# Kernel tuning notes

Measured on AMD Instinct MI355X. Metric: run time of the kernel, lower is better.

Reference implementation:

```python
import jax, jax.numpy as jnp
import numpy as np

RADII = (0.4, 0.8, 1.2)
SIGMA2 = 2.0 * 0.2 ** 2   # Gaussian shell-density bandwidth
ALPHA = 0.3               # keras LeakyReLU default
EPS = 1e-3                # keras BatchNormalization default epsilon


def _n_coeffs(L):
    return sum((2 * l + 1) ** 2 for l in range(L + 1))


def _pullback_idx(L):
    # flat index of Wigner block entry (m, n=0) for each SH coeff (l, m)
    idx, off = [], 0
    for l in range(L + 1):
        d = 2 * l + 1
        idx += [off + m * d + l for m in range(d)]
        off += d * d
    return np.asarray(idx, dtype=np.int32)


def setup_inputs() -> dict:
    key = jax.random.key(0)
    ks = jax.random.split(key, 20)
    B, N, Q, S = 64, 2048, 1024, 512
    T = [_n_coeffs(l) for l in (5, 4, 3)]  # 286, 165, 84
    f32 = jnp.float32

    def nrm(k, shape, scale=1.0):
        return jax.random.normal(ks[k], shape, dtype=f32) * scale

    dirs = nrm(1, (3, S, 3))
    dirs = dirs / jnp.linalg.norm(dirs, axis=-1, keepdims=True)
    z = lambda n: jnp.zeros((n,), f32)
    o = lambda n: jnp.ones((n,), f32)
    return {
        "x": nrm(0, (B, N, 3)),
        "shell_dirs": dirs,                                   # [3, 512, 3]
        "A_sh": nrm(2, (36, S), 1.0 / np.sqrt(S)),            # SH projection (l_max=5)
        "D_eval0": nrm(3, (Q, T[0]), 1.0 / np.sqrt(T[0])),    # Wigner eval bases
        "D_eval1": nrm(4, (Q, T[1]), 1.0 / np.sqrt(T[1])),
        "D_eval2": nrm(5, (Q, T[2]), 1.0 / np.sqrt(T[2])),
        "D_coef1": nrm(6, (T[1], Q), 1.0 / np.sqrt(Q)),       # Wigner coeff (projection) bases
        "D_coef2": nrm(7, (T[2], Q), 1.0 / np.sqrt(Q)),
        "D_coef_last": nrm(8, (T[2], Q), 1.0 / np.sqrt(Q)),
        "W0": nrm(9, (3, 16), 1.0 / np.sqrt(3)), "b0": z(16),
        "W1": nrm(10, (16, 32), 0.25), "b1": z(32),
        "W2": nrm(11, (32, 64), 1.0 / np.sqrt(32)), "b2": z(64),
        "g0": o(16), "be0": z(16),
        "g1": o(32), "be1": z(32),
        "g2": o(64), "be2": z(64),
        "Wfc1": nrm(12, (256, 512), 1.0 / 16.0), "bfc1": z(512),
        "gfc1": o(512), "befc1": z(512),
        "Wfc2": nrm(13, (512, 256), 1.0 / np.sqrt(512)), "bfc2": z(256),
        "gfc2": o(256), "befc2": z(256),
        "Wout": nrm(14, (256, 40), 1.0 / 16.0), "bout": z(40),
    }


def _bn(y, g, b, axes):
    m = jnp.mean(y, axis=axes, keepdims=True)
    v = jnp.var(y, axis=axes, keepdims=True)
    return (y - m) * jax.lax.rsqrt(v + EPS) * g + b


def reference(x, shell_dirs, A_sh, D_eval0, D_eval1, D_eval2,
              D_coef1, D_coef2, D_coef_last,
              W0, b0, W1, b1, W2, b2,
              g0, be0, g1, be1, g2, be2,
              Wfc1, bfc1, gfc1, befc1, Wfc2, bfc2, gfc2, befc2,
              Wout, bout):
    B = x.shape[0]
    # --- sphere_shell_embedding: Gaussian shell density -> SH coeffs per shell ---
    xn2 = jnp.sum(x * x, -1)[..., None]                 # [B,N,1]
    sh = []
    for i, r in enumerate(RADII):
        c = r * shell_dirs[i]                           # [S,3]
        d2 = xn2 + jnp.sum(c * c, -1) - 2.0 * (x @ c.T)  # [B,N,S]
        f = jnp.mean(jnp.exp(-d2 / SIGMA2), axis=1)      # [B,S]
        sh.append(f @ A_sh.T)                            # [B,36]
    sh = jnp.stack(sh, axis=-1)                          # [B,36,3] shells as channels
    # --- S2_to_SO3_pullback: Y_lm -> D^l_{m,0} column of Wigner blocks ---
    idx = jnp.asarray(_pullback_idx(5))
    y = jnp.zeros((B, 286, 3), sh.dtype).at[:, idx, :].set(sh)
    # --- layer 0: SO3Conv (per-coeff channel mix) + WignerEval + BN + LReLU + WignerCoeffs ---
    y = jnp.einsum('btc,cu->btu', y, W0) + b0
    y = jnp.einsum('qt,btu->bqu', D_eval0, y)            # [B,1024,16]
    y = jax.nn.leaky_relu(_bn(y, g0, be0, (0, 1)), ALPHA)
    y = jnp.einsum('tq,bqu->btu', D_coef1, y)            # [B,165,16]
    # --- layer 1 ---
    y = jnp.einsum('btc,cu->btu', y, W1) + b1
    y = jnp.einsum('qt,btu->bqu', D_eval1, y)            # [B,1024,32]
    y = jax.nn.leaky_relu(_bn(y, g1, be1, (0, 1)), ALPHA)
    y = jnp.einsum('tq,bqu->btu', D_coef2, y)            # [B,84,32]
    # --- layer 2 ---
    y = jnp.einsum('btc,cu->btu', y, W2) + b2
    y = jnp.einsum('qt,btu->bqu', D_eval2, y)            # [B,1024,64]
    y = jax.nn.leaky_relu(_bn(y, g2, be2, (0, 1)), ALPHA)
    y = jnp.einsum('tq,bqu->btu', D_coef_last, y)        # [B,84,64]
    # --- degree-wise norms (rotation-invariant pooling), l_max=3 blocks ---
    offs, sizes = (0, 1, 10, 35), (1, 9, 25, 49)
    feats = jnp.concatenate(
        [jnp.linalg.norm(y[:, o:o + s, :], axis=1, keepdims=True)
         for o, s in zip(offs, sizes)], axis=1)          # [B,4,64]
    h = feats.reshape(B, -1)                             # [B,256]
    # --- MLP head (dropout = identity at inference) ---
    h = jax.nn.relu(_bn(h @ Wfc1 + bfc1, gfc1, befc1, (0,)))
    h = jax.nn.relu(_bn(h @ Wfc2 + bfc2, gfc2, befc2, (0,)))
    return jax.nn.softmax(h @ Wout + bout, axis=-1)
```

## Files before the change

### kernel.cpp

```cpp
#include <hip/hip_runtime.h>
#include <hip/hip_bf16.h>

#define BB 64
#define NN 2048
#define QQ 1024
#define SS 512
#define NCH 8
#define PREPB 609
#define QKN3 4

__device__ const int PIDX[36] = {
    0, 2, 5, 8, 12, 17, 22, 27, 32, 38, 45, 52, 59, 66, 73, 80,
    88, 97, 106, 115, 124, 133, 142, 151, 160,
    170, 181, 192, 203, 214, 225, 236, 247, 258, 269, 280};

__global__ __launch_bounds__(256) void k_preshell(
    const float* __restrict__ De0, const float* __restrict__ De1, const float* __restrict__ De2,
    float* __restrict__ Dg0t, float* __restrict__ rs0,
    float* __restrict__ Det1, float* __restrict__ Det2,
    float* __restrict__ stats,
    const float* __restrict__ x, const float* __restrict__ dirs, float* __restrict__ pbuf) {
    __shared__ float tile[32][33];
    __shared__ float4 lx[NN / NCH];
    int blk = blockIdx.x, tid = threadIdx.x;
    if (blk < PREPB) {
        int r = tid >> 5, c = tid & 31;
        if (blk < 192) {
            int tq = blk & 31, tt = blk >> 5;
            int q0 = tq * 32, t0 = tt * 32;
            for (int rr = r; rr < 32; rr += 8) {
                int t = t0 + c;
                tile[rr][c] = (t < 165) ? De1[(q0 + rr) * 165 + t] : 0.f;
            }
            __syncthreads();
            for (int rr = r; rr < 32; rr += 8) {
                int t = t0 + rr;
                if (t < 165) Det1[t * QQ + q0 + c] = tile[c][rr];
            }
        } else if (blk < 288) {
            int i = blk - 192;
            int tq = i & 31, tt = i >> 5;
            int q0 = tq * 32, t0 = tt * 32;
            for (int rr = r; rr < 32; rr += 8) {
                int t = t0 + c;
                tile[rr][c] = (t < 84) ? De2[(q0 + rr) * 84 + t] : 0.f;
            }
            __syncthreads();
            for (int rr = r; rr < 32; rr += 8) {
                int t = t0 + rr;
                if (t < 84) Det2[t * QQ + q0 + c] = tile[c][rr];
            }
        } else if (blk < 352) {
            int i = blk - 288;
            int tq = i & 31, tj = i >> 5;
            int q0 = tq * 32, j0 = tj * 32;
            for (int rr = r; rr < 32; rr += 8) {
                int j = j0 + c;
                tile[rr][c] = (j < 36) ? De0[(q0 + rr) * 286 + PIDX[j]] : 0.f;
            }
            __syncthreads();
            for (int rr = r; rr < 32; rr += 8) {
                int j = j0 + rr;
                if (j < 36) Dg0t[j * QQ + q0 + c] = tile[c][rr];
            }
        } else if (blk < 608) {
            int w = tid >> 6, lane = tid & 63;
            int q = (blk - 352) * 4 + w;
            float s = 0.f;
#pragma unroll
            for (int p = 0; p < 5; p++) {
                int idx = lane + p * 64;
                if (idx < 286) s += De0[q * 286 + idx];
            }
#pragma unroll
            for (int o = 32; o > 0; o >>= 1) s += __shfl_xor(s, o, 64);
            if (lane == 0) rs0[q] = s;
        } else {
            if (tid < 224) stats[tid] = 0.f;
        }
        return;
    }
    int s = blk - PREPB;
    int b = s & 63, rest = s >> 6;
    int shell = rest % 3, zc = rest / 3;
    const float KL = 18.033688011112042f;
    const float* xb = x + ((size_t)b * NN + zc * (NN / NCH)) * 3;
    for (int n = tid; n < NN / NCH; n += 256) {
        float X = xb[n * 3 + 0];
        float Y = xb[n * 3 + 1];
        float Z = xb[n * 3 + 2];
        lx[n] = make_float4(X, Y, Z, -KL * (X * X + Y * Y + Z * Z));
    }
    __syncthreads();
    float r = (shell == 0) ? 0.4f : ((shell == 1) ? 0.8f : 1.2f);
    int s0 = tid, s1 = tid + 256;
    float cx0 = r * dirs[(shell * SS + s0) * 3 + 0];
    float cy0 = r * dirs[(shell * SS + s0) * 3 + 1];
    float cz0 = r * dirs[(shell * SS + s0) * 3 + 2];
    float cx1 = r * dirs[(shell * SS + s1) * 3 + 0];
    float cy1 = r * dirs[(shell * SS + s1) * 3 + 1];
    float cz1 = r * dirs[(shell * SS + s1) * 3 + 2];
    float base0 = -KL * (cx0 * cx0 + cy0 * cy0 + cz0 * cz0);
    float base1 = -KL * (cx1 * cx1 + cy1 * cy1 + cz1 * cz1);
    float cxs0 = 2.f * KL * cx0, cys0 = 2.f * KL * cy0, czs0 = 2.f * KL * cz0;
    float cxs1 = 2.f * KL * cx1, cys1 = 2.f * KL * cy1, czs1 = 2.f * KL * cz1;
    float a0 = 0.f, a1 = 0.f;
#pragma unroll 8
    for (int n = 0; n < NN / NCH; n++) {
        float4 p = lx[n];
        a0 += __builtin_amdgcn_exp2f(fmaf(cxs0, p.x, fmaf(cys0, p.y, fmaf(czs0, p.z, p.w + base0))));
        a1 += __builtin_amdgcn_exp2f(fmaf(cxs1, p.x, fmaf(cys1, p.y, fmaf(czs1, p.z, p.w + base1))));
    }
    float* o = pbuf + ((size_t)(zc * 3 + shell) * BB + b) * SS;
    o[s0] = a0;
    o[s1] = a1;
}

__global__ __launch_bounds__(1024) void k_sh(const float* __restrict__ pbuf,
                                             const float* __restrict__ A_sh,
                                             const float* __restrict__ W0,
                                             float* __restrict__ lm_ws) {
    __shared__ float lf[3][SS];
    __shared__ float lsh[36][3];
    int b = blockIdx.x, tid = threadIdx.x;
    for (int i = tid; i < 3 * SS; i += 1024) {
        int c = i / SS, s = i % SS;
        float v = 0.f;
#pragma unroll
        for (int zc = 0; zc < NCH; zc++) v += pbuf[((size_t)(zc * 3 + c) * BB + b) * SS + s];
        lf[c][s] = v * (1.0f / NN);
    }
    __syncthreads();
    int w = tid >> 6, lane = tid & 63;
    for (int p = w; p < 108; p += 16) {
        int j = p / 3, c = p % 3;
        const float* As = A_sh + j * SS;
        float a = 0.f;
#pragma unroll
        for (int k = 0; k < 8; k++) a = fmaf(lf[c][lane + 64 * k], As[lane + 64 * k], a);
#pragma unroll
        for (int o = 32; o > 0; o >>= 1) a += __shfl_xor(a, o, 64);
        if (lane == 0) lsh[j][c] = a;
    }
    __syncthreads();
    for (int i = tid; i < 576; i += 1024) {
        int j = i >> 4, u = i & 15;
        float m = 0.f;
#pragma unroll
        for (int c = 0; c < 3; c++) m = fmaf(lsh[j][c], W0[c * 16 + u], m);
        lm_ws[b * 576 + i] = m;
    }
}

__global__ __launch_bounds__(256) void k_eval0q(const float* __restrict__ lm_ws,
                                                const float* __restrict__ b0,
                                                const float* __restrict__ Dg0t,
                                                const float* __restrict__ rs0,
                                                float* __restrict__ yq, float* __restrict__ stats) {
    __shared__ float llm[576];
    __shared__ float lred[4][32];
    int qc = blockIdx.x, b = blockIdx.y, tid = threadIdx.x;
    for (int i = tid; i < 576; i += 256) llm[i] = lm_ws[b * 576 + i];
    __syncthreads();
    int q = qc * 256 + tid;
    float acc[16];
#pragma unroll
    for (int u = 0; u < 16; u++) acc[u] = 0.f;
#pragma unroll 4
    for (int j = 0; j < 36; j++) {
        float d = Dg0t[j * QQ + q];
#pragma unroll
        for (int u = 0; u < 16; u++) acc[u] = fmaf(d, llm[j * 16 + u], acc[u]);
    }
    float rb = rs0[q];
#pragma unroll
    for (int u = 0; u < 16; u++) acc[u] = fmaf(b0[u], rb, acc[u]);
#pragma unroll
    for (int u = 0; u < 16; u++) yq[((size_t)b * 16 + u) * QQ + q] = acc[u];
    int lane = tid & 63, w = tid >> 6;
#pragma unroll
    for (int u = 0; u < 16; u++) {
        float v = acc[u], v2 = acc[u] * acc[u];
#pragma unroll
        for (int o = 32; o > 0; o >>= 1) {
            v += __shfl_xor(v, o, 64);
            v2 += __shfl_xor(v2, o, 64);
        }
        if (lane == 0) { lred[w][u] = v; lred[w][16 + u] = v2; }
    }
    __syncthreads();
    if (tid < 32) atomicAdd(&stats[tid], lred[0][tid] + lred[1][tid] + lred[2][tid] + lred[3][tid]);
}

template <int TT, int UU, int QKN>
__global__ __launch_bounds__(256) void k_coefG(const float* __restrict__ yq,
                                               const float* __restrict__ Dc,
                                               const float* __restrict__ stats,
                                               const float* __restrict__ g,
                                               const float* __restrict__ be,
                                               float* __restrict__ part) {
    constexpr int KC = QQ / QKN;
    __shared__ float lA[32][68];
    __shared__ float lB[32][68];
    __shared__ float lsu[UU], ltu[UU];
    int mt = blockIdx.x, nt = blockIdx.y, qk = blockIdx.z, tid = threadIdx.x;
    int m0 = mt * 64, n0 = nt * 64, k0 = qk * KC;
    if (tid < UU) {
        const float inv = 1.0f / (BB * QQ);
        float mm = stats[tid] * inv;
        float var = stats[UU + tid] * inv - mm * mm;
        float s = g[tid] * rsqrtf(fmaxf(var, 0.f) + 1e-3f);
        lsu[tid] = s;
        ltu[tid] = be[tid] - mm * s;
    }
    __syncthreads();
    int r = tid >> 2;
    int f = (tid & 3) * 4;
    bool mok = (m0 + r) < TT;
    const float* arow = Dc + (size_t)(mok ? (m0 + r) : 0) * QQ;
    const float* brow = yq + (size_t)(n0 + r) * QQ;
    float su = lsu[(n0 + r) % UU], tu = ltu[(n0 + r) % UU];
    int tg = tid >> 4, ug = tid & 15;
    float acc[4][4];
#pragma unroll
    for (int i = 0; i < 4; i++)
#pragma unroll
        for (int j = 0; j < 4; j++) acc[i][j] = 0.f;
    for (int kb = 0; kb < KC; kb += 32) {
        int kg = k0 + kb;
#pragma unroll
        for (int p = 0; p < 2; p++) {
            int ko = f + p * 16;
            float4 a4 = make_float4(0.f, 0.f, 0.f, 0.f);
            if (mok) a4 = *(const float4*)(arow + kg + ko);
            float4 b4 = *(const float4*)(brow + kg + ko);
#pragma unroll
            for (int i = 0; i < 4; i++) {
                float v = fmaf((&b4.x)[i], su, tu);
                lA[ko + i][r] = (&a4.x)[i];
                lB[ko + i][r] = (v > 0.f) ? v : 0.3f * v;
            }
        }
        __syncthreads();
#pragma unroll 2
        for (int kk = 0; kk < 32; kk++) {
            float4 a4 = *(const float4*)&lA[kk][tg * 4];
            float4 b4 = *(const float4*)&lB[kk][ug * 4];
#pragma unroll
            for (int i = 0; i < 4; i++) {
                float av = (&a4.x)[i];
                acc[i][0] = fmaf(av, b4.x, acc[i][0]);
                acc[i][1] = fmaf(av, b4.y, acc[i][1]);
                acc[i][2] = fmaf(av, b4.z, acc[i][2]);
                acc[i][3] = fmaf(av, b4.w, acc[i][3]);
            }
        }
        __syncthreads();
    }
    int n = n0 + ug * 4;
    int b = n / UU, u0 = n % UU;
#pragma unroll
    for (int i = 0; i < 4; i++) {
        int t = m0 + tg * 4 + i;
        if (t < TT)
            *(float4*)&part[(((size_t)qk * BB + b) * TT + t) * UU + u0] =
                make_float4(acc[i][0], acc[i][1], acc[i][2], acc[i][3]);
    }
}

template <int N>
__global__ __launch_bounds__(256) void k_red(const float* __restrict__ part, float* __restrict__ yt) {
    int i = (blockIdx.x * 256 + threadIdx.x) * 4;
    if (i >= N) return;
    float4 s = make_float4(0.f, 0.f, 0.f, 0.f);
#pragma unroll
    for (int k = 0; k < 8; k++) {
        float4 v = *(const float4*)&part[(size_t)k * N + i];
        s.x += v.x; s.y += v.y; s.z += v.z; s.w += v.w;
    }
    *(float4*)&yt[i] = s;
}

template <int TT, int CC, int UU>
__global__ __launch_bounds__(256) void k_eval(const float* __restrict__ yt,
                                              const float* __restrict__ W, const float* __restrict__ bias,
                                              const float* __restrict__ Det,
                                              float* __restrict__ yq, float* __restrict__ stats) {
    __shared__ float lyt[TT * CC];
    __shared__ float lym[TT * 16];
    __shared__ float lred[4][32];
    int qc = blockIdx.x, b = blockIdx.y, uz = blockIdx.z * 16, tid = threadIdx.x;
    for (int i = tid; i < TT * CC; i += 256) lyt[i] = yt[(size_t)b * TT * CC + i];
    __syncthreads();
    for (int e = tid; e < TT * 16; e += 256) {
        int t = e >> 4, ul = e & 15, u = uz + ul;
        float m = bias[u];
#pragma unroll
        for (int c = 0; c < CC; c++) m = fmaf(lyt[t * CC + c], W[c * UU + u], m);
        lym[e] = m;
    }
    __syncthreads();
    int q = qc * 256 + tid;
    float acc[16];
#pragma unroll
    for (int u = 0; u < 16; u++) acc[u] = 0.f;
#pragma unroll 4
    for (int t = 0; t < TT; t++) {
        float d = Det[t * QQ + q];
#pragma unroll
        for (int u = 0; u < 16; u++) acc[u] = fmaf(d, lym[t * 16 + u], acc[u]);
    }
#pragma unroll
    for (int u = 0; u < 16; u++) yq[((size_t)b * UU + uz + u) * QQ + q] = acc[u];
    int lane = tid & 63, w = tid >> 6;
#pragma unroll
    for (int u = 0; u < 16; u++) {
        float v = acc[u], v2 = acc[u] * acc[u];
#pragma unroll
        for (int o = 32; o > 0; o >>= 1) {
            v += __shfl_xor(v, o, 64);
            v2 += __shfl_xor(v2, o, 64);
        }
        if (lane == 0) { lred[w][u] = v; lred[w][16 + u] = v2; }
    }
    __syncthreads();
    if (tid < 32) {
        float s = lred[0][tid] + lred[1][tid] + lred[2][tid] + lred[3][tid];
        int idx = (tid < 16) ? (uz + tid) : (UU + uz + tid - 16);
        atomicAdd(&stats[idx], s);
    }
}

__global__ __launch_bounds__(256) void k_norms(const float* __restrict__ part, float* __restrict__ ht0) {
    __shared__ float ly[84 * 64];
    int b = blockIdx.x, tid = threadIdx.x;
    for (int i = tid; i < 84 * 64; i += 256) {
        float v = 0.f;
#pragma unroll
        for (int k = 0; k < QKN3; k++) v += part[(size_t)k * (BB * 84 * 64) + b * (84 * 64) + i];
        ly[i] = v;
    }
    __syncthreads();
    int blk = tid >> 6, u = tid & 63;
    const int offs[4] = {0, 1, 10, 35};
    const int ends[4] = {1, 10, 35, 84};
    float a = 0.f;
    for (int t = offs[blk]; t < ends[blk]; t++) {
        float v = ly[t * 64 + u];
        a = fmaf(v, v, a);
    }
    ht0[(blk * 64 + u) * BB + b] = sqrtf(fmaxf(a, 0.f));
}

template <int K, int J>
__global__ __launch_bounds__(512) void k_fc(const float* __restrict__ in, const float* __restrict__ W,
                                            const float* __restrict__ bias, const float* __restrict__ g,
                                            const float* __restrict__ be, float* __restrict__ out) {
    __shared__ float red[8][64];
    int j = blockIdx.x;
    int b = threadIdx.x & 63, kq = threadIdx.x >> 6;
    constexpr int KS = K / 8;
    int kbeg = kq * KS;
    float a0 = 0.f, a1 = 0.f, a2 = 0.f, a3 = 0.f;
#pragma unroll 4
    for (int k = kbeg; k < kbeg + KS; k += 4) {
        a0 = fmaf(in[k * BB + b], W[(size_t)k * J + j], a0);
        a1 = fmaf(in[(k + 1) * BB + b], W[(size_t)(k + 1) * J + j], a1);
        a2 = fmaf(in[(k + 2) * BB + b], W[(size_t)(k + 2) * J + j], a2);
        a3 = fmaf(in[(k + 3) * BB + b], W[(size_t)(k + 3) * J + j], a3);
    }
    red[kq][b] = (a0 + a1) + (a2 + a3);
    __syncthreads();
    if (kq == 0) {
        float acc = bias[j];
#pragma unroll
        for (int i = 0; i < 8; i++) acc += red[i][b];
        float s1 = acc, s2 = acc * acc;
#pragma unroll
        for (int o = 32; o > 0; o >>= 1) {
            s1 += __shfl_xor(s1, o, 64);
            s2 += __shfl_xor(s2, o, 64);
        }
        float m = s1 * (1.0f / 64.f);
        float var = s2 * (1.0f / 64.f) - m * m;
        float sc = g[j] * rsqrtf(fmaxf(var, 0.f) + 1e-3f);
        float v = (acc - m) * sc + be[j];
        out[j * BB + b] = fmaxf(v, 0.f);
    }
}

__global__ __launch_bounds__(256) void k_out(const float* __restrict__ ht2, const float* __restrict__ Wout,
                                             const float* __restrict__ bout, float* __restrict__ outp) {
    __shared__ float red[4][64];
    __shared__ float sm[64];
    int b = blockIdx.x;
    int o = threadIdx.x & 63, kq = threadIdx.x >> 6;
    float a0 = 0.f, a1 = 0.f, a2 = 0.f, a3 = 0.f;
    int kbeg = kq * 64;
    if (o < 40) {
#pragma unroll 4
        for (int k = kbeg; k < kbeg + 64; k += 4) {
            a0 = fmaf(ht2[k * BB + b], Wout[k * 40 + o], a0);
            a1 = fmaf(ht2[(k + 1) * BB + b], Wout[(k + 1) * 40 + o], a1);
            a2 = fmaf(ht2[(k + 2) * BB + b], Wout[(k + 2) * 40 + o], a2);
            a3 = fmaf(ht2[(k + 3) * BB + b], Wout[(k + 3) * 40 + o], a3);
        }
    }
    red[kq][o] = (a0 + a1) + (a2 + a3);
    __syncthreads();
    if (kq == 0) {
        float acc = red[0][o] + red[1][o] + red[2][o] + red[3][o] + ((o < 40) ? bout[o] : 0.f);
        sm[o] = (o < 40) ? acc : -3.0e38f;
        __syncthreads();
        for (int s = 32; s > 0; s >>= 1) {
            if (o < s) sm[o] = fmaxf(sm[o], sm[o + s]);
            __syncthreads();
        }
        float m = sm[0];
        __syncthreads();
        const float L2E = 1.4426950408889634f;
        float e = (o < 40) ? exp2f((acc - m) * L2E) : 0.f;
        sm[o] = e;
        __syncthreads();
        for (int s = 32; s > 0; s >>= 1) {
            if (o < s) sm[o] += sm[o + s];
            __syncthreads();
        }
        if (o < 40) outp[b * 40 + o] = e / sm[0];
    }
}

#define OFF_PBUF 0
#define OFF_DG0T 786432
#define OFF_RS0 823296
#define OFF_DET1 824320
#define OFF_DET2 993280
#define OFF_LM 1079296
#define OFF_YQ 1116160
#define OFF_PART 5310464
#define OFF_YT 6686720
#define OFF_HT0 7027712
#define OFF_HT1 7044096
#define OFF_HT2 7076864
#define OFF_STATS 7093248

extern "C" void kernel_launch(void* const* d_in, const int* in_sizes, int n_in,
                              void* d_out, int out_size, void* d_ws, size_t ws_size,
                              hipStream_t stream) {
    const float* x = (const float*)d_in[0];
    const float* shell_dirs = (const float*)d_in[1];
    const float* A_sh = (const float*)d_in[2];
    const float* D_eval0 = (const float*)d_in[3];
    const float* D_eval1 = (const float*)d_in[4];
    const float* D_eval2 = (const float*)d_in[5];
    const float* D_coef1 = (const float*)d_in[6];
    const float* D_coef2 = (const float*)d_in[7];
    const float* D_coef_last = (const float*)d_in[8];
    const float* W0 = (const float*)d_in[9];
    const float* b0 = (const float*)d_in[10];
    const float* W1 = (const float*)d_in[11];
    const float* b1 = (const float*)d_in[12];
    const float* W2 = (const float*)d_in[13];
    const float* b2 = (const float*)d_in[14];
    const float* g0 = (const float*)d_in[15];
    const float* be0 = (const float*)d_in[16];
    const float* g1 = (const float*)d_in[17];
    const float* be1 = (const float*)d_in[18];
    const float* g2 = (const float*)d_in[19];
    const float* be2 = (const float*)d_in[20];
    const float* Wfc1 = (const float*)d_in[21];
    const float* bfc1 = (const float*)d_in[22];
    const float* gfc1 = (const float*)d_in[23];
    const float* befc1 = (const float*)d_in[24];
    const float* Wfc2 = (const float*)d_in[25];
    const float* bfc2 = (const float*)d_in[26];
    const float* gfc2 = (const float*)d_in[27];
    const float* befc2 = (const float*)d_in[28];
    const float* Wout = (const float*)d_in[29];
    const float* bout = (const float*)d_in[30];
    float* out = (float*)d_out;

    float* ws = (float*)d_ws;
    float* pbuf = ws + OFF_PBUF;
    float* Dg0t = ws + OFF_DG0T;
    float* rs0 = ws + OFF_RS0;
    float* Det1 = ws + OFF_DET1;
    float* Det2 = ws + OFF_DET2;
    float* lm_ws = ws + OFF_LM;
    float* yq = ws + OFF_YQ;
    float* part = ws + OFF_PART;
    float* yt1 = ws + OFF_YT;
    float* yt2 = yt1 + 168960;
    float* ht0 = ws + OFF_HT0;
    float* ht1 = ws + OFF_HT1;
    float* ht2 = ws + OFF_HT2;
    float* stats = ws + OFF_STATS;
    float* stats0 = stats;
    float* stats1 = stats + 32;
    float* stats2 = stats + 96;

    k_preshell<<<PREPB + BB * 3 * NCH, 256, 0, stream>>>(
        D_eval0, D_eval1, D_eval2, Dg0t, rs0, Det1, Det2, stats, x, shell_dirs, pbuf);
    k_sh<<<BB, 1024, 0, stream>>>(pbuf, A_sh, W0, lm_ws);
    k_eval0q<<<dim3(4, BB), 256, 0, stream>>>(lm_ws, b0, Dg0t, rs0, yq, stats0);
    k_coefG<165, 16, 8><<<dim3(3, 16, 8), 256, 0, stream>>>(yq, D_coef1, stats0, g0, be0, part);
    k_red<168960><<<165, 256, 0, stream>>>(part, yt1);
    k_eval<165, 16, 32><<<dim3(4, BB, 2), 256, 0, stream>>>(yt1, W1, b1, Det1, yq, stats1);
    k_coefG<84, 32, 8><<<dim3(2, 32, 8), 256, 0, stream>>>(yq, D_coef2, stats1, g1, be1, part);
    k_red<172032><<<168, 256, 0, stream>>>(part, yt2);
    k_eval<84, 32, 64><<<dim3(4, BB, 4), 256, 0, stream>>>(yt2, W2, b2, Det2, yq, stats2);
    k_coefG<84, 64, QKN3><<<dim3(2, 64, QKN3), 256, 0, stream>>>(yq, D_coef_last, stats2, g2, be2, part);
    k_norms<<<BB, 256, 0, stream>>>(part, ht0);
    k_fc<256, 512><<<512, 512, 0, stream>>>(ht0, Wfc1, bfc1, gfc1, befc1, ht1);
    k_fc<512, 256><<<256, 512, 0, stream>>>(ht1, Wfc2, bfc2, gfc2, befc2, ht2);
    k_out<<<BB, 256, 0, stream>>>(ht2, Wout, bout, out);
}
```

Before: 335.3 us.

## Fuse SH projection into eval0, fold split-K reductions into eval, restructure shell kernel

Each shell-density block now computes all three shells for a point chunk, reusing the staged points, with the point dimension split 16 ways instead of 8. The SH projection kernel is merged into the layer-0 eval kernel, and the split-K reduction kernels are removed by summing partials inside the eval kernels' shared-memory load. This cuts three launches and their intermediate buffers. In exchange, the SH projection is recomputed by each of the 4 q-chunk blocks, and the eval kernels read 8 partial buffers redundantly across q and channel blocks.

```diff
diff --git a/kernel.cpp b/kernel.cpp
--- a/kernel.cpp
+++ b/kernel.cpp
@@ -5,7 +5,7 @@
 #define NN 2048
 #define QQ 1024
 #define SS 512
-#define NCH 8
+#define NCH 16
 #define PREPB 609
 #define QKN3 4
 
@@ -80,9 +80,8 @@
         }
         return;
     }
-    int s = blk - PREPB;
-    int b = s & 63, rest = s >> 6;
-    int shell = rest % 3, zc = rest / 3;
+    int idx = blk - PREPB;
+    int b = idx & 63, zc = idx >> 6;
     const float KL = 18.033688011112042f;
     const float* xb = x + ((size_t)b * NN + zc * (NN / NCH)) * 3;
     for (int n = tid; n < NN / NCH; n += 256) {
@@ -92,38 +91,56 @@
         lx[n] = make_float4(X, Y, Z, -KL * (X * X + Y * Y + Z * Z));
     }
     __syncthreads();
-    float r = (shell == 0) ? 0.4f : ((shell == 1) ? 0.8f : 1.2f);
-    int s0 = tid, s1 = tid + 256;
-    float cx0 = r * dirs[(shell * SS + s0) * 3 + 0];
-    float cy0 = r * dirs[(shell * SS + s0) * 3 + 1];
-    float cz0 = r * dirs[(shell * SS + s0) * 3 + 2];
-    float cx1 = r * dirs[(shell * SS + s1) * 3 + 0];
-    float cy1 = r * dirs[(shell * SS + s1) * 3 + 1];
-    float cz1 = r * dirs[(shell * SS + s1) * 3 + 2];
-    float base0 = -KL * (cx0 * cx0 + cy0 * cy0 + cz0 * cz0);
-    float base1 = -KL * (cx1 * cx1 + cy1 * cy1 + cz1 * cz1);
-    float cxs0 = 2.f * KL * cx0, cys0 = 2.f * KL * cy0, czs0 = 2.f * KL * cz0;
-    float cxs1 = 2.f * KL * cx1, cys1 = 2.f * KL * cy1, czs1 = 2.f * KL * cz1;
-    float a0 = 0.f, a1 = 0.f;
-#pragma unroll 8
+    float cxs[3][2], cys[3][2], czs[3][2], bas[3][2];
+#pragma unroll
+    for (int i = 0; i < 3; i++) {
+        float r = (i == 0) ? 0.4f : ((i == 1) ? 0.8f : 1.2f);
+#pragma unroll
+        for (int h = 0; h < 2; h++) {
+            int s = tid + h * 256;
+            float cx = r * dirs[(i * SS + s) * 3 + 0];
+            float cy = r * dirs[(i * SS + s) * 3 + 1];
+            float cz = r * dirs[(i * SS + s) * 3 + 2];
+            bas[i][h] = -KL * (cx * cx + cy * cy + cz * cz);
+            cxs[i][h] = 2.f * KL * cx;
+            cys[i][h] = 2.f * KL * cy;
+            czs[i][h] = 2.f * KL * cz;
+        }
+    }
+    float acc[3][2];
+#pragma unroll
+    for (int i = 0; i < 3; i++) { acc[i][0] = 0.f; acc[i][1] = 0.f; }
+#pragma unroll 4
     for (int n = 0; n < NN / NCH; n++) {
         float4 p = lx[n];
-        a0 += __builtin_amdgcn_exp2f(fmaf(cxs0, p.x, fmaf(cys0, p.y, fmaf(czs0, p.z, p.w + base0))));
-        a1 += __builtin_amdgcn_exp2f(fmaf(cxs1, p.x, fmaf(cys1, p.y, fmaf(czs1, p.z, p.w + base1))));
-    }
-    float* o = pbuf + ((size_t)(zc * 3 + shell) * BB + b) * SS;
-    o[s0] = a0;
-    o[s1] = a1;
-}
-
-__global__ __launch_bounds__(1024) void k_sh(const float* __restrict__ pbuf,
-                                             const float* __restrict__ A_sh,
-                                             const float* __restrict__ W0,
-                                             float* __restrict__ lm_ws) {
+#pragma unroll
+        for (int i = 0; i < 3; i++)
+#pragma unroll
+            for (int h = 0; h < 2; h++)
+                acc[i][h] += __builtin_amdgcn_exp2f(
+                    fmaf(cxs[i][h], p.x, fmaf(cys[i][h], p.y, fmaf(czs[i][h], p.z, p.w + bas[i][h]))));
+    }
+#pragma unroll
+    for (int i = 0; i < 3; i++) {
+        float* o = pbuf + ((size_t)(zc * 3 + i) * BB + b) * SS;
+        o[tid] = acc[i][0];
+        o[tid + 256] = acc[i][1];
+    }
+}
+
+__global__ __launch_bounds__(256) void k_eval0(const float* __restrict__ pbuf,
+                                               const float* __restrict__ A_sh,
+                                               const float* __restrict__ W0,
+                                               const float* __restrict__ b0,
+                                               const float* __restrict__ Dg0t,
+                                               const float* __restrict__ rs0,
+                                               float* __restrict__ yq, float* __restrict__ stats) {
     __shared__ float lf[3][SS];
     __shared__ float lsh[36][3];
-    int b = blockIdx.x, tid = threadIdx.x;
-    for (int i = tid; i < 3 * SS; i += 1024) {
+    __shared__ float llm[576];
+    __shared__ float lred[4][32];
+    int qc = blockIdx.x, b = blockIdx.y, tid = threadIdx.x;
+    for (int i = tid; i < 3 * SS; i += 256) {
         int c = i / SS, s = i % SS;
         float v = 0.f;
 #pragma unroll
@@ -132,7 +149,7 @@
     }
     __syncthreads();
     int w = tid >> 6, lane = tid & 63;
-    for (int p = w; p < 108; p += 16) {
+    for (int p = w; p < 108; p += 4) {
         int j = p / 3, c = p % 3;
         const float* As = A_sh + j * SS;
         float a = 0.f;
@@ -143,24 +160,13 @@
         if (lane == 0) lsh[j][c] = a;
     }
     __syncthreads();
-    for (int i = tid; i < 576; i += 1024) {
+    for (int i = tid; i < 576; i += 256) {
         int j = i >> 4, u = i & 15;
         float m = 0.f;
 #pragma unroll
         for (int c = 0; c < 3; c++) m = fmaf(lsh[j][c], W0[c * 16 + u], m);
-        lm_ws[b * 576 + i] = m;
-    }
-}
-
-__global__ __launch_bounds__(256) void k_eval0q(const float* __restrict__ lm_ws,
-                                                const float* __restrict__ b0,
-                                                const float* __restrict__ Dg0t,
-                                                const float* __restrict__ rs0,
-                                                float* __restrict__ yq, float* __restrict__ stats) {
-    __shared__ float llm[576];
-    __shared__ float lred[4][32];
-    int qc = blockIdx.x, b = blockIdx.y, tid = threadIdx.x;
-    for (int i = tid; i < 576; i += 256) llm[i] = lm_ws[b * 576 + i];
+        llm[i] = m;
+    }
     __syncthreads();
     int q = qc * 256 + tid;
     float acc[16];
@@ -177,7 +183,6 @@
     for (int u = 0; u < 16; u++) acc[u] = fmaf(b0[u], rb, acc[u]);
 #pragma unroll
     for (int u = 0; u < 16; u++) yq[((size_t)b * 16 + u) * QQ + q] = acc[u];
-    int lane = tid & 63, w = tid >> 6;
 #pragma unroll
     for (int u = 0; u < 16; u++) {
         float v = acc[u], v2 = acc[u] * acc[u];
@@ -268,21 +273,8 @@
     }
 }
 
-template <int N>
-__global__ __launch_bounds__(256) void k_red(const float* __restrict__ part, float* __restrict__ yt) {
-    int i = (blockIdx.x * 256 + threadIdx.x) * 4;
-    if (i >= N) return;
-    float4 s = make_float4(0.f, 0.f, 0.f, 0.f);
-#pragma unroll
-    for (int k = 0; k < 8; k++) {
-        float4 v = *(const float4*)&part[(size_t)k * N + i];
-        s.x += v.x; s.y += v.y; s.z += v.z; s.w += v.w;
-    }
-    *(float4*)&yt[i] = s;
-}
-
-template <int TT, int CC, int UU>
-__global__ __launch_bounds__(256) void k_eval(const float* __restrict__ yt,
+template <int TT, int CC, int UU, int QKN>
+__global__ __launch_bounds__(256) void k_eval(const float* __restrict__ part,
                                               const float* __restrict__ W, const float* __restrict__ bias,
                                               const float* __restrict__ Det,
                                               float* __restrict__ yq, float* __restrict__ stats) {
@@ -290,7 +282,12 @@
     __shared__ float lym[TT * 16];
     __shared__ float lred[4][32];
     int qc = blockIdx.x, b = blockIdx.y, uz = blockIdx.z * 16, tid = threadIdx.x;
-    for (int i = tid; i < TT * CC; i += 256) lyt[i] = yt[(size_t)b * TT * CC + i];
+    for (int i = tid; i < TT * CC; i += 256) {
+        float v = 0.f;
+#pragma unroll
+        for (int k = 0; k < QKN; k++) v += part[(size_t)k * (BB * TT * CC) + (size_t)b * TT * CC + i];
+        lyt[i] = v;
+    }
     __syncthreads();
     for (int e = tid; e < TT * 16; e += 256) {
         int t = e >> 4, ul = e & 15, u = uz + ul;
@@ -431,18 +428,15 @@
 }
 
 #define OFF_PBUF 0
-#define OFF_DG0T 786432
-#define OFF_RS0 823296
-#define OFF_DET1 824320
-#define OFF_DET2 993280
-#define OFF_LM 1079296
-#define OFF_YQ 1116160
-#define OFF_PART 5310464
-#define OFF_YT 6686720
-#define OFF_HT0 7027712
-#define OFF_HT1 7044096
-#define OFF_HT2 7076864
-#define OFF_STATS 7093248
+#define OFF_DG0T 1572864
+#define OFF_RS0 1609728
+#define OFF_DET1 1610752
+#define OFF_DET2 1779712
+#define OFF_YQ 1865728
+#define OFF_HT0 6060032
+#define OFF_HT1 6076416
+#define OFF_HT2 6109184
+#define OFF_STATS 6125568
 
 extern "C" void kernel_launch(void* const* d_in, const int* in_sizes, int n_in,
                               void* d_out, int out_size, void* d_ws, size_t ws_size,
@@ -482,15 +476,12 @@
 
     float* ws = (float*)d_ws;
     float* pbuf = ws + OFF_PBUF;
+    float* part = ws + OFF_PBUF;
     float* Dg0t = ws + OFF_DG0T;
     float* rs0 = ws + OFF_RS0;
     float* Det1 = ws + OFF_DET1;
     float* Det2 = ws + OFF_DET2;
-    float* lm_ws = ws + OFF_LM;
     float* yq = ws + OFF_YQ;
-    float* part = ws + OFF_PART;
-    float* yt1 = ws + OFF_YT;
-    float* yt2 = yt1 + 168960;
     float* ht0 = ws + OFF_HT0;
     float* ht1 = ws + OFF_HT1;
     float* ht2 = ws + OFF_HT2;
@@ -499,16 +490,13 @@
     float* stats1 = stats + 32;
     float* stats2 = stats + 96;
 
-    k_preshell<<<PREPB + BB * 3 * NCH, 256, 0, stream>>>(
+    k_preshell<<<PREPB + BB * NCH, 256, 0, stream>>>(
         D_eval0, D_eval1, D_eval2, Dg0t, rs0, Det1, Det2, stats, x, shell_dirs, pbuf);
-    k_sh<<<BB, 1024, 0, stream>>>(pbuf, A_sh, W0, lm_ws);
-    k_eval0q<<<dim3(4, BB), 256, 0, stream>>>(lm_ws, b0, Dg0t, rs0, yq, stats0);
+    k_eval0<<<dim3(4, BB), 256, 0, stream>>>(pbuf, A_sh, W0, b0, Dg0t, rs0, yq, stats0);
     k_coefG<165, 16, 8><<<dim3(3, 16, 8), 256, 0, stream>>>(yq, D_coef1, stats0, g0, be0, part);
-    k_red<168960><<<165, 256, 0, stream>>>(part, yt1);
-    k_eval<165, 16, 32><<<dim3(4, BB, 2), 256, 0, stream>>>(yt1, W1, b1, Det1, yq, stats1);
+    k_eval<165, 16, 32, 8><<<dim3(4, BB, 2), 256, 0, stream>>>(part, W1, b1, Det1, yq, stats1);
     k_coefG<84, 32, 8><<<dim3(2, 32, 8), 256, 0, stream>>>(yq, D_coef2, stats1, g1, be1, part);
-    k_red<172032><<<168, 256, 0, stream>>>(part, yt2);
-    k_eval<84, 32, 64><<<dim3(4, BB, 4), 256, 0, stream>>>(yt2, W2, b2, Det2, yq, stats2);
+    k_eval<84, 32, 64, 8><<<dim3(4, BB, 4), 256, 0, stream>>>(part, W2, b2, Det2, yq, stats2);
     k_coefG<84, 64, QKN3><<<dim3(2, 64, QKN3), 256, 0, stream>>>(yq, D_coef_last, stats2, g2, be2, part);
     k_norms<<<BB, 256, 0, stream>>>(part, ht0);
     k_fc<256, 512><<<512, 512, 0, stream>>>(ht0, Wfc1, bfc1, gfc1, befc1, ht1);
```

Result: slower. 345.7 us (+3.1%).
